# Kernel optimization log

Measured on AMD Instinct MI355X. Metric: run time of the kernel, lower is better.

## Reference

```python
import jax, jax.numpy as jnp
import numpy as np

# geomloss SamplesLoss(loss='sinkhorn', p=2, blur=0.05):
#   cost C(x,y) = |x-y|^2 / 2, entropic eps = blur**p = 0.0025,
#   debiased divergence S = OT(x,y) - 0.5*OT(x,x) - 0.5*OT(y,y)
EPS = 0.05 ** 2          # blur**p
N_ITERS = 50             # fixed log-domain Sinkhorn iterations


def _cost(x, y):
    # x: [N,3], y: [M,3] -> [N,M] halved squared euclidean distance
    x2 = jnp.sum(x * x, axis=-1)
    y2 = jnp.sum(y * y, axis=-1)
    return 0.5 * (x2[:, None] + y2[None, :] - 2.0 * (x @ y.T))


def _ot_eps(x, y):
    # Entropic OT with uniform weights, log-domain Sinkhorn.
    N, M = x.shape[0], y.shape[0]
    logN = float(np.log(N))
    logM = float(np.log(M))
    C = _cost(x, y)  # [N,M]
    f0 = jnp.zeros((N,), dtype=x.dtype)
    g0 = jnp.zeros((M,), dtype=x.dtype)

    def step(carry, _):
        f, g = carry
        f = -EPS * (jax.nn.logsumexp((g[None, :] - C) / EPS, axis=1) - logM)
        g = -EPS * (jax.nn.logsumexp((f[:, None] - C) / EPS, axis=0) - logN)
        return (f, g), None

    (f, g), _ = jax.lax.scan(step, (f0, g0), None, length=N_ITERS)
    # OT cost at (approximate) optimal dual potentials
    return jnp.mean(f) + jnp.mean(g)


def _sinkhorn_div(x, y):
    # debiased Sinkhorn divergence per sample
    return _ot_eps(x, y) - 0.5 * _ot_eps(x, x) - 0.5 * _ot_eps(y, y)


def setup_inputs() -> dict:
    key = jax.random.key(0)
    k1, k2 = jax.random.split(key)
    B, N = 8, 2048
    pcs1 = jax.random.uniform(k1, (B, N, 3), dtype=jnp.float32)
    pcs2 = jax.random.uniform(k2, (B, N, 3), dtype=jnp.float32)
    return {"pcs1": pcs1, "pcs2": pcs2}


def reference(pcs1, pcs2):
    # mean over batch of per-sample Sinkhorn divergences
    losses = jax.vmap(_sinkhorn_div)(pcs1, pcs2)  # [B]
    return jnp.mean(losses)
```

## Files before the change

### kernel.cpp

```cpp
#include <hip/hip_runtime.h>

#ifndef __has_builtin
#define __has_builtin(x) 0
#endif

__device__ __forceinline__ float fexp2(float x) {
#if __has_builtin(__builtin_amdgcn_exp2f)
  return __builtin_amdgcn_exp2f(x);
#else
  return exp2f(x);
#endif
}
__device__ __forceinline__ float flog2(float x) {
#if __has_builtin(__builtin_amdgcn_logf)
  return __builtin_amdgcn_logf(x);
#else
  return log2f(x);
#endif
}

typedef float    f32x4 __attribute__((ext_vector_type(4)));
typedef unsigned int u32x2 __attribute__((ext_vector_type(2)));
typedef unsigned int u32x4 __attribute__((ext_vector_type(4)));
typedef _Float16 f16x4 __attribute__((ext_vector_type(4)));

__device__ __forceinline__ f32x4 mfma16x16x16(f16x4 a, f16x4 b, f32x4 c) {
#if __has_builtin(__builtin_amdgcn_mfma_f32_16x16x16_f16)
  return __builtin_amdgcn_mfma_f32_16x16x16_f16(a, b, c, 0, 0, 0);
#else
  return __builtin_amdgcn_mfma_f32_16x16x16f16(a, b, c, 0, 0, 0);
#endif
}

namespace {
constexpr int NPTS = 2048;
constexpr int HALF = 1024;
constexpr int NPROB = 24;
constexpr int WGS_PER_PROB = 64;
constexpr int THREADS = 256;
constexpr int NPASS = 100;
constexpr float KS  = 1.44269504088896340736f / 0.0025f;
constexpr float HKS = 0.5f * KS;
constexpr float NEG_EPS_LN2 = -0.0025f * 0.69314718055994530942f;
constexpr float LOG2N = 11.0f;
}

__device__ __forceinline__ void split2h(float v, float& h, float& m) {
  h = (float)(_Float16)v;
  m = (float)(_Float16)(v - h);
}
__device__ __forceinline__ void split3h(float v, float& h, float& m, float& l) {
  h = (float)(_Float16)v;
  float r1 = v - h;
  m = (float)(_Float16)r1;
  l = r1 - m;
}
__device__ __forceinline__ unsigned pkh(float a, float b) {
  unsigned short ab = __builtin_bit_cast(unsigned short, (_Float16)a);
  unsigned short bb = __builtin_bit_cast(unsigned short, (_Float16)b);
  return (unsigned)ab | ((unsigned)bb << 16);
}

__global__ void __launch_bounds__(THREADS, 4) sink_mfma(
    const float* __restrict__ p1, const float* __restrict__ p2,
    float* __restrict__ fm, float* __restrict__ fs,
    float* __restrict__ gm, float* __restrict__ gs, int t)
{
  __shared__ u32x4 Bfr[HALF * 2];
  __shared__ float wmax[4];

  const int w   = blockIdx.x;
  const int p   = w >> 6;
  const int r_  = w & 63;
  const int blk = r_ & 31;
  const int h   = r_ >> 5;
  const int b    = p / 3;
  const int kind = p - 3 * b;
  const float* X = (kind == 2 ? p2 : p1) + b * (NPTS * 3);
  const float* Y = (kind == 1 ? p1 : p2) + b * (NPTS * 3);

  const bool even = (t & 1) == 0;
  const float* tgt = even ? X : Y;
  const float* src = even ? Y : X;
  const float* pmA = even ? gm : fm;
  const float* psA = even ? gs : fs;
  float* omA = even ? fm : gm;
  float* osA = even ? fs : gs;

  const int tid  = threadIdx.x;
  const int lane = tid & 63;
  const int wv   = tid >> 6;
  const int l15  = lane & 15;
  const int kb   = lane >> 4;

  float am = -1e30f;
  #pragma unroll
  for (int i = 0; i < HALF / THREADS; ++i) {
    int jl = tid + THREADS * i;
    int jg = HALF * h + jl;
    float sx = src[3 * jg + 0], sy = src[3 * jg + 1], sz = src[3 * jg + 2];
    float q2 = HKS * (sx * sx + sy * sy + sz * sz);
    float A;
    if (t == 0) {
      A = -q2;
    } else {
      float m0 = pmA[(p * 2 + 0) * NPTS + jg];
      float m1 = pmA[(p * 2 + 1) * NPTS + jg];
      float c0 = psA[(p * 2 + 0) * NPTS + jg];
      float c1 = psA[(p * 2 + 1) * NPTS + jg];
      float M = fmaxf(m0, m1);
      float S = fmaf(c0, fexp2(m0 - M), c1 * fexp2(m1 - M));
      A = LOG2N - M - flog2(fmaxf(S, 1e-38f));
    }
    am = fmaxf(am, A + q2);
    float shx, smx, shy, smy, shz, smz, Ah, Am, Al;
    split2h(KS * sx, shx, smx);
    split2h(KS * sy, shy, smy);
    split2h(KS * sz, shz, smz);
    split3h(A, Ah, Am, Al);
    unsigned wx = pkh(shx, smx), wy = pkh(shy, smy), wz = pkh(shz, smz);
    Bfr[jl * 2 + 0] = (u32x4){wx, wx, wy, wy};
    Bfr[jl * 2 + 1] = (u32x4){wz, wz, pkh(Ah, Am), pkh(Al, 0.f)};
  }

  #pragma unroll
  for (int off = 1; off <= 32; off <<= 1) am = fmaxf(am, __shfl_xor(am, off));
  if (lane == 0) wmax[wv] = am;

  const int rowbase = blk * 64 + wv * 16;
  const int r = rowbase + l15;
  float tx = tgt[3 * r + 0], ty = tgt[3 * r + 1], tz = tgt[3 * r + 2];
  float thx, tmx, thy, tmy, thz, tmz;
  split2h(tx, thx, tmx);
  split2h(ty, thy, tmy);
  split2h(tz, thz, tmz);
  u32x2 areg;
  if (kb == 0)      { areg = (u32x2){pkh(thx, thx), pkh(tmx, tmx)}; }
  else if (kb == 1) { areg = (u32x2){pkh(thy, thy), pkh(tmy, tmy)}; }
  else if (kb == 2) { areg = (u32x2){pkh(thz, thz), pkh(tmz, tmz)}; }
  else              { areg = (u32x2){pkh(1.f, 1.f), pkh(1.f, 0.f)}; }
  const f16x4 afrag = __builtin_bit_cast(f16x4, areg);
  const float Bv = -HKS * (tx * tx + ty * ty + tz * tz);

  __syncthreads();

  const float Amax = fmaxf(fmaxf(wmax[0], wmax[1]), fmaxf(wmax[2], wmax[3]));
  const float Bp0 = __shfl(Bv, kb * 4 + 0) - Amax;
  const float Bp1 = __shfl(Bv, kb * 4 + 1) - Amax;
  const float Bp2 = __shfl(Bv, kb * 4 + 2) - Amax;
  const float Bp3 = __shfl(Bv, kb * 4 + 3) - Amax;
  const f32x4 cin = {Bp0, Bp1, Bp2, Bp3};

  const u32x2* bptr = (const u32x2*)Bfr + (l15 * 4 + kb);
  float s0 = 0.f, s1 = 0.f, s2 = 0.f, s3 = 0.f;

  #pragma unroll 4
  for (int tile = 0; tile < HALF / 16; ++tile) {
    u32x2 braw = *bptr; bptr += 64;
    f16x4 bfrag = __builtin_bit_cast(f16x4, braw);
    f32x4 d = mfma16x16x16(afrag, bfrag, cin);
    s0 += fexp2(d.x);
    s1 += fexp2(d.y);
    s2 += fexp2(d.z);
    s3 += fexp2(d.w);
  }

  #pragma unroll
  for (int off = 1; off <= 8; off <<= 1) {
    s0 += __shfl_xor(s0, off);
    s1 += __shfl_xor(s1, off);
    s2 += __shfl_xor(s2, off);
    s3 += __shfl_xor(s3, off);
  }

  if (l15 == 0) {
    float* om = omA + (p * 2 + h) * NPTS;
    float* os = osA + (p * 2 + h) * NPTS;
    int r0 = rowbase + kb * 4;
    om[r0 + 0] = -Bp0; os[r0 + 0] = s0;
    om[r0 + 1] = -Bp1; os[r0 + 1] = s1;
    om[r0 + 2] = -Bp2; os[r0 + 2] = s2;
    om[r0 + 3] = -Bp3; os[r0 + 3] = s3;
  }
}

__global__ void __launch_bounds__(256) sink_partial(
    const float* __restrict__ fm, const float* __restrict__ fs,
    const float* __restrict__ gm, const float* __restrict__ gs,
    const float* __restrict__ p1, const float* __restrict__ p2,
    double* __restrict__ part)
{
  __shared__ double wsum[4];
  const int tid = threadIdx.x;
  const int blk = blockIdx.x;
  const int PER_SIDE = NPROB * NPTS;
  double acc = 0.0;
  #pragma unroll
  for (int k = 0; k < 4; ++k) {
    int idx = blk * 1024 + k * 256 + tid;
    int side = idx >= PER_SIDE;
    int rem  = idx - side * PER_SIDE;
    int p = rem >> 11;
    int i = rem & (NPTS - 1);
    const float* mA = side ? gm : fm;
    const float* sA = side ? gs : fs;
    float m0 = mA[(p * 2 + 0) * NPTS + i], m1 = mA[(p * 2 + 1) * NPTS + i];
    float c0 = sA[(p * 2 + 0) * NPTS + i], c1 = sA[(p * 2 + 1) * NPTS + i];
    float M = fmaxf(m0, m1);
    float S = fmaf(c0, fexp2(m0 - M), c1 * fexp2(m1 - M));
    int b = p / 3, kd = p - 3 * b;
    const float* rows = side ? (kd == 1 ? p1 : p2) : (kd == 2 ? p2 : p1);
    const float* pt = rows + b * (NPTS * 3) + 3 * i;
    float B = -HKS * (pt[0] * pt[0] + pt[1] * pt[1] + pt[2] * pt[2]);
    float val = NEG_EPS_LN2 * (M + B + flog2(fmaxf(S, 1e-38f)) - LOG2N);
    double wgt = (kd == 0) ? 1.0 : -0.5;
    acc += wgt * (double)val;
  }
  #pragma unroll
  for (int off = 1; off <= 32; off <<= 1) acc += __shfl_xor(acc, off);
  if ((tid & 63) == 0) wsum[tid >> 6] = acc;
  __syncthreads();
  if (tid == 0) part[blk] = ((wsum[0] + wsum[1]) + (wsum[2] + wsum[3]));
}

__global__ void __launch_bounds__(64) sink_reduce(
    const double* __restrict__ part, float* __restrict__ out)
{
  const int tid = threadIdx.x;
  double acc = part[tid] + (tid < 32 ? part[64 + tid] : 0.0);
  #pragma unroll
  for (int off = 1; off <= 32; off <<= 1) acc += __shfl_xor(acc, off);
  if (tid == 0) out[0] = (float)(acc / (8.0 * 2048.0));
}

extern "C" void kernel_launch(void* const* d_in, const int* in_sizes, int n_in,
                              void* d_out, int out_size, void* d_ws, size_t ws_size,
                              hipStream_t stream)
{
  const float* p1 = (const float*)d_in[0];
  const float* p2 = (const float*)d_in[1];
  float* fm = (float*)d_ws;
  float* fs = fm + NPROB * 2 * NPTS;
  float* gm = fs + NPROB * 2 * NPTS;
  float* gs = gm + NPROB * 2 * NPTS;
  double* part = (double*)(gs + NPROB * 2 * NPTS);

  for (int t = 0; t < NPASS; ++t) {
    sink_mfma<<<dim3(NPROB * WGS_PER_PROB), dim3(THREADS), 0, stream>>>(
        p1, p2, fm, fs, gm, gs, t);
  }
  sink_partial<<<dim3(96), dim3(256), 0, stream>>>(fm, fs, gm, gs, p1, p2, part);
  sink_reduce<<<dim3(1), dim3(64), 0, stream>>>(part, (float*)d_out);
}
```

Baseline: 2.049 ms.

## Split source points into four chunks per problem to raise workgroup count

Generalizes the source-axis split from two halves to NS chunks, picking four when the workspace is large enough. This doubles the grid to 3072 workgroups, each doing half the MFMA tiles, and raises the occupancy hint in launch bounds. The aim is better CU utilization and latency hiding on a launch-bound iterative kernel. In exchange there is more partial (max, sum) state to merge in the next pass and in the final reduction, plus per-workgroup setup overhead and dynamic shared memory.

```diff
diff --git a/kernel.cpp b/kernel.cpp
--- a/kernel.cpp
+++ b/kernel.cpp
@@ -34,9 +34,7 @@
 
 namespace {
 constexpr int NPTS = 2048;
-constexpr int HALF = 1024;
 constexpr int NPROB = 24;
-constexpr int WGS_PER_PROB = 64;
 constexpr int THREADS = 256;
 constexpr int NPASS = 100;
 constexpr float KS  = 1.44269504088896340736f / 0.0025f;
@@ -61,17 +59,20 @@
   return (unsigned)ab | ((unsigned)bb << 16);
 }
 
-__global__ void __launch_bounds__(THREADS, 4) sink_mfma(
+template <int NS>
+__global__ void __launch_bounds__(THREADS, 8) sink_mfma(
     const float* __restrict__ p1, const float* __restrict__ p2,
     float* __restrict__ fm, float* __restrict__ fs,
     float* __restrict__ gm, float* __restrict__ gs, int t)
 {
-  __shared__ u32x4 Bfr[HALF * 2];
-  __shared__ float wmax[4];
+  constexpr int SRC = NPTS / NS;
+  extern __shared__ char smem[];
+  u32x4* Bfr  = (u32x4*)smem;
+  float* wmax = (float*)(smem + SRC * 32);
 
   const int w   = blockIdx.x;
-  const int p   = w >> 6;
-  const int r_  = w & 63;
+  const int p   = w / (32 * NS);
+  const int r_  = w - p * (32 * NS);
   const int blk = r_ & 31;
   const int h   = r_ >> 5;
   const int b    = p / 3;
@@ -95,21 +96,24 @@
 
   float am = -1e30f;
   #pragma unroll
-  for (int i = 0; i < HALF / THREADS; ++i) {
+  for (int i = 0; i < SRC / THREADS; ++i) {
     int jl = tid + THREADS * i;
-    int jg = HALF * h + jl;
+    int jg = SRC * h + jl;
     float sx = src[3 * jg + 0], sy = src[3 * jg + 1], sz = src[3 * jg + 2];
     float q2 = HKS * (sx * sx + sy * sy + sz * sz);
     float A;
     if (t == 0) {
       A = -q2;
     } else {
-      float m0 = pmA[(p * 2 + 0) * NPTS + jg];
-      float m1 = pmA[(p * 2 + 1) * NPTS + jg];
-      float c0 = psA[(p * 2 + 0) * NPTS + jg];
-      float c1 = psA[(p * 2 + 1) * NPTS + jg];
-      float M = fmaxf(m0, m1);
-      float S = fmaf(c0, fexp2(m0 - M), c1 * fexp2(m1 - M));
+      float M = pmA[(p * NS + 0) * NPTS + jg];
+      #pragma unroll
+      for (int q = 1; q < NS; ++q)
+        M = fmaxf(M, pmA[(p * NS + q) * NPTS + jg]);
+      float S = 0.f;
+      #pragma unroll
+      for (int q = 0; q < NS; ++q)
+        S = fmaf(psA[(p * NS + q) * NPTS + jg],
+                 fexp2(pmA[(p * NS + q) * NPTS + jg] - M), S);
       A = LOG2N - M - flog2(fmaxf(S, 1e-38f));
     }
     am = fmaxf(am, A + q2);
@@ -155,7 +159,7 @@
   float s0 = 0.f, s1 = 0.f, s2 = 0.f, s3 = 0.f;
 
   #pragma unroll 4
-  for (int tile = 0; tile < HALF / 16; ++tile) {
+  for (int tile = 0; tile < SRC / 16; ++tile) {
     u32x2 braw = *bptr; bptr += 64;
     f16x4 bfrag = __builtin_bit_cast(f16x4, braw);
     f32x4 d = mfma16x16x16(afrag, bfrag, cin);
@@ -174,8 +178,8 @@
   }
 
   if (l15 == 0) {
-    float* om = omA + (p * 2 + h) * NPTS;
-    float* os = osA + (p * 2 + h) * NPTS;
+    float* om = omA + (p * NS + h) * NPTS;
+    float* os = osA + (p * NS + h) * NPTS;
     int r0 = rowbase + kb * 4;
     om[r0 + 0] = -Bp0; os[r0 + 0] = s0;
     om[r0 + 1] = -Bp1; os[r0 + 1] = s1;
@@ -188,7 +192,7 @@
     const float* __restrict__ fm, const float* __restrict__ fs,
     const float* __restrict__ gm, const float* __restrict__ gs,
     const float* __restrict__ p1, const float* __restrict__ p2,
-    double* __restrict__ part)
+    double* __restrict__ part, int ns)
 {
   __shared__ double wsum[4];
   const int tid = threadIdx.x;
@@ -204,10 +208,12 @@
     int i = rem & (NPTS - 1);
     const float* mA = side ? gm : fm;
     const float* sA = side ? gs : fs;
-    float m0 = mA[(p * 2 + 0) * NPTS + i], m1 = mA[(p * 2 + 1) * NPTS + i];
-    float c0 = sA[(p * 2 + 0) * NPTS + i], c1 = sA[(p * 2 + 1) * NPTS + i];
-    float M = fmaxf(m0, m1);
-    float S = fmaf(c0, fexp2(m0 - M), c1 * fexp2(m1 - M));
+    float M = mA[(p * ns + 0) * NPTS + i];
+    for (int q = 1; q < ns; ++q) M = fmaxf(M, mA[(p * ns + q) * NPTS + i]);
+    float S = 0.f;
+    for (int q = 0; q < ns; ++q)
+      S = fmaf(sA[(p * ns + q) * NPTS + i],
+               fexp2(mA[(p * ns + q) * NPTS + i] - M), S);
     int b = p / 3, kd = p - 3 * b;
     const float* rows = side ? (kd == 1 ? p1 : p2) : (kd == 2 ? p2 : p1);
     const float* pt = rows + b * (NPTS * 3) + 3 * i;
@@ -239,16 +245,30 @@
 {
   const float* p1 = (const float*)d_in[0];
   const float* p2 = (const float*)d_in[1];
+
+  const size_t elems4 = (size_t)NPROB * 4 * NPTS;
+  const size_t need4  = 4 * elems4 * sizeof(float) + 96 * sizeof(double);
+  const int ns = (ws_size >= need4) ? 4 : 2;
+  const size_t elems = (size_t)NPROB * ns * NPTS;
+
   float* fm = (float*)d_ws;
-  float* fs = fm + NPROB * 2 * NPTS;
-  float* gm = fs + NPROB * 2 * NPTS;
-  float* gs = gm + NPROB * 2 * NPTS;
-  double* part = (double*)(gs + NPROB * 2 * NPTS);
+  float* fs = fm + elems;
+  float* gm = fs + elems;
+  float* gs = gm + elems;
+  double* part = (double*)(gs + elems);
+
+  const int grid = NPROB * 32 * ns;
+  const int shmem = (NPTS / ns) * 32 + 16;
 
   for (int t = 0; t < NPASS; ++t) {
-    sink_mfma<<<dim3(NPROB * WGS_PER_PROB), dim3(THREADS), 0, stream>>>(
-        p1, p2, fm, fs, gm, gs, t);
-  }
-  sink_partial<<<dim3(96), dim3(256), 0, stream>>>(fm, fs, gm, gs, p1, p2, part);
+    if (ns == 4)
+      sink_mfma<4><<<dim3(grid), dim3(THREADS), shmem, stream>>>(
+          p1, p2, fm, fs, gm, gs, t);
+    else
+      sink_mfma<2><<<dim3(grid), dim3(THREADS), shmem, stream>>>(
+          p1, p2, fm, fs, gm, gs, t);
+  }
+  sink_partial<<<dim3(96), dim3(256), 0, stream>>>(fm, fs, gm, gs, p1, p2,
+                                                   part, ns);
   sink_reduce<<<dim3(1), dim3(64), 0, stream>>>(part, (float*)d_out);
 }
```

Result: faster. 2.001 ms (-2.3%).
